# Kernel optimization log

Measured on AMD Instinct MI355X. Metric: run time of the kernel, lower is better.

## Reference

```python
import jax, jax.numpy as jnp
import numpy as np

N_EXPERTS = 6
TOP_K = 2
AUX_COEFF = 0.01
W_SCALE = 0.02  # keep activations in a sane range with random weights


def setup_inputs() -> dict:
    key = jax.random.key(0)
    k1, k2, k3, k4 = jax.random.split(key, 4)
    B, T, D, H = 4, 2048, 1024, 4096
    x = jax.random.normal(k1, (B, T, D), dtype=jnp.float32)
    w_router = jax.random.normal(k2, (D, N_EXPERTS), dtype=jnp.float32) * W_SCALE
    w1 = jax.random.normal(k3, (N_EXPERTS, D, H), dtype=jnp.float32) * W_SCALE
    w2 = jax.random.normal(k4, (N_EXPERTS, H, D), dtype=jnp.float32) * W_SCALE
    return {"x": x, "w_router": w_router, "w1": w1, "w2": w2}


def reference(x, w_router, w1, w2):
    B, T, D = x.shape
    x_flat = x.reshape(-1, D)                              # (N, D)
    router_logits = x_flat @ w_router                      # (N, E)
    router_probs = jax.nn.softmax(router_logits, axis=-1)
    top_probs, top_idx = jax.lax.top_k(router_probs, TOP_K)  # (N, K)
    top_probs = top_probs / jnp.sum(top_probs, axis=-1, keepdims=True)
    # combine weights per (token, expert): sum over k slots hitting expert e
    onehot = jax.nn.one_hot(top_idx, N_EXPERTS, dtype=x.dtype)  # (N, K, E)
    comb = jnp.einsum('nke,nk->ne', onehot, top_probs)          # (N, E)
    out = jnp.zeros_like(x_flat)
    for e in range(N_EXPERTS):
        h = jax.nn.gelu(x_flat @ w1[e], approximate=False)      # (N, H)
        out = out + comb[:, e:e + 1] * (h @ w2[e])              # (N, D)
    tokens_per_expert = jnp.mean(router_probs, axis=0)          # (E,)
    uniform = jnp.full_like(tokens_per_expert, 1.0 / N_EXPERTS)
    aux_loss = AUX_COEFF * jnp.mean((tokens_per_expert - uniform) ** 2)
    return out.reshape(B, T, D), aux_loss
```

## Files before the change

kernel.cpp:

```cpp
#include <hip/hip_runtime.h>

#define N_TOK 8192
#define DDIM  1024
#define HDIM  4096
#define NEXP  6
#define RBLOCKS (N_TOK / 4)
#define SBLOCKS 32

typedef unsigned short ushort_t;
typedef __bf16 bf16_t;
typedef bf16_t bf16x8 __attribute__((ext_vector_type(8)));
typedef float f32x4 __attribute__((ext_vector_type(4)));

typedef const __attribute__((address_space(1))) void* gptr_t;
typedef __attribute__((address_space(3))) void* lptr_t;

__device__ __forceinline__ void g2l16(const void* g, void* l) {
    __builtin_amdgcn_global_load_lds((gptr_t)g, (lptr_t)l, 16, 0, 0);
}

__device__ __forceinline__ ushort_t f2bf(float f) {
    unsigned int u = __float_as_uint(f);
    unsigned int r = (u + 0x7FFFu + ((u >> 16) & 1u)) >> 16;
    return (ushort_t)r;
}

__global__ void convert_x_kernel(const float* __restrict__ x, ushort_t* __restrict__ xb) {
    size_t i = (size_t)(blockIdx.x * 256 + threadIdx.x) * 8;
    float4 a = *(const float4*)(x + i);
    float4 b = *(const float4*)(x + i + 4);
    union { ushort_t u[8]; uint4 v; } o;
    o.u[0] = f2bf(a.x); o.u[1] = f2bf(a.y); o.u[2] = f2bf(a.z); o.u[3] = f2bf(a.w);
    o.u[4] = f2bf(b.x); o.u[5] = f2bf(b.y); o.u[6] = f2bf(b.z); o.u[7] = f2bf(b.w);
    *(uint4*)(xb + i) = o.v;
}

__global__ void transpose_bf16_kernel(const float* __restrict__ src, ushort_t* __restrict__ dst,
                                      int R, int C) {
    __shared__ float tile[32][33];
    size_t msz = (size_t)R * C;
    src += (size_t)blockIdx.z * msz;
    dst += (size_t)blockIdx.z * msz;
    int c0 = blockIdx.x * 32, r0 = blockIdx.y * 32;
    int tx = threadIdx.x & 31, ty = threadIdx.x >> 5;
#pragma unroll
    for (int i = 0; i < 4; ++i)
        tile[ty + 8 * i][tx] = src[(size_t)(r0 + ty + 8 * i) * C + c0 + tx];
    __syncthreads();
#pragma unroll
    for (int i = 0; i < 4; ++i)
        dst[(size_t)(c0 + ty + 8 * i) * R + r0 + tx] = f2bf(tile[tx][ty + 8 * i]);
}

__global__ void router_kernel(const float* __restrict__ x, const float* __restrict__ wr,
                              int* __restrict__ tok_e, float* __restrict__ tok_w,
                              float* __restrict__ part_p, int* __restrict__ part_c) {
    __shared__ float bsum[NEXP];
    __shared__ int bcnt[NEXP];
    int wid = threadIdx.x >> 6, l = threadIdx.x & 63;
    if (threadIdx.x < NEXP) { bsum[threadIdx.x] = 0.f; bcnt[threadIdx.x] = 0; }
    __syncthreads();
    int t = blockIdx.x * 4 + wid;
    const float* xr = x + (size_t)t * DDIM;
    float acc[NEXP] = {0.f, 0.f, 0.f, 0.f, 0.f, 0.f};
#pragma unroll
    for (int c = 0; c < 4; ++c) {
        int k0 = c * 256 + l * 4;
        float4 xv = *(const float4*)(xr + k0);
        float wv[24];
#pragma unroll
        for (int q = 0; q < 6; ++q)
            *(float4*)(wv + 4 * q) = *(const float4*)(wr + (size_t)k0 * NEXP + 4 * q);
        float xa[4] = {xv.x, xv.y, xv.z, xv.w};
#pragma unroll
        for (int r = 0; r < 4; ++r)
#pragma unroll
            for (int e = 0; e < NEXP; ++e) acc[e] += xa[r] * wv[r * NEXP + e];
    }
#pragma unroll
    for (int e = 0; e < NEXP; ++e)
#pragma unroll
        for (int d = 32; d >= 1; d >>= 1) acc[e] += __shfl_xor(acc[e], d);
    if (l == 0) {
        float m = acc[0];
#pragma unroll
        for (int e = 1; e < NEXP; ++e) m = fmaxf(m, acc[e]);
        float p[NEXP], s = 0.f;
#pragma unroll
        for (int e = 0; e < NEXP; ++e) { p[e] = expf(acc[e] - m); s += p[e]; }
        float inv = 1.0f / s;
#pragma unroll
        for (int e = 0; e < NEXP; ++e) p[e] *= inv;
        int i1 = 0; float b1 = p[0];
#pragma unroll
        for (int e = 1; e < NEXP; ++e) if (p[e] > b1) { b1 = p[e]; i1 = e; }
        int i2 = -1; float b2 = -1.f;
#pragma unroll
        for (int e = 0; e < NEXP; ++e) if (e != i1 && p[e] > b2) { b2 = p[e]; i2 = e; }
        float swn = 1.0f / (b1 + b2);
        tok_e[2 * t] = i1; tok_e[2 * t + 1] = i2;
        tok_w[2 * t] = b1 * swn; tok_w[2 * t + 1] = b2 * swn;
        atomicAdd(&bcnt[i1], 1);
        atomicAdd(&bcnt[i2], 1);
#pragma unroll
        for (int e = 0; e < NEXP; ++e) atomicAdd(&bsum[e], p[e]);
    }
    __syncthreads();
    if (threadIdx.x < NEXP) {
        part_p[(size_t)blockIdx.x * NEXP + threadIdx.x] = bsum[threadIdx.x];
        part_c[(size_t)blockIdx.x * NEXP + threadIdx.x] = bcnt[threadIdx.x];
    }
}

__global__ void finalize_kernel(const float* __restrict__ part_p, const int* __restrict__ part_c,
                                int* __restrict__ counts, int* __restrict__ offs,
                                float* __restrict__ aux_out) {
    __shared__ float redp[NEXP][4];
    __shared__ int redc[NEXP][4];
    int tid = threadIdx.x, wid = tid >> 6, l = tid & 63;
    float myp[NEXP] = {0.f, 0.f, 0.f, 0.f, 0.f, 0.f};
    int myc[NEXP] = {0, 0, 0, 0, 0, 0};
    for (int b = tid; b < RBLOCKS; b += 256) {
#pragma unroll
        for (int e = 0; e < NEXP; ++e) {
            myp[e] += part_p[(size_t)b * NEXP + e];
            myc[e] += part_c[(size_t)b * NEXP + e];
        }
    }
#pragma unroll
    for (int e = 0; e < NEXP; ++e) {
#pragma unroll
        for (int d = 32; d >= 1; d >>= 1) {
            myp[e] += __shfl_xor(myp[e], d);
            myc[e] += __shfl_xor(myc[e], d);
        }
        if (l == 0) { redp[e][wid] = myp[e]; redc[e][wid] = myc[e]; }
    }
    __syncthreads();
    if (tid == 0) {
        int o = 0;
        float s = 0.f;
        for (int e = 0; e < NEXP; ++e) {
            int c = redc[e][0] + redc[e][1] + redc[e][2] + redc[e][3];
            float ps = redp[e][0] + redp[e][1] + redp[e][2] + redp[e][3];
            counts[e] = c;
            offs[e] = o;
            o += c;
            float d = ps / (float)N_TOK - (1.0f / 6.0f);
            s += d * d;
        }
        offs[NEXP] = o;
        aux_out[0] = 0.01f * (s / 6.0f);
    }
}

__global__ void scatter_kernel(const int* __restrict__ tok_e, const float* __restrict__ tok_w,
                               const int* __restrict__ offs, int* __restrict__ cursors,
                               int* __restrict__ slot_token, float* __restrict__ slot_w) {
    __shared__ int lcnt[NEXP], lbase[NEXP];
    int tid = threadIdx.x;
    if (tid < NEXP) lcnt[tid] = 0;
    __syncthreads();
    int t = blockIdx.x * 256 + tid;
    int e0 = tok_e[2 * t], e1 = tok_e[2 * t + 1];
    int r0 = atomicAdd(&lcnt[e0], 1);
    int r1 = atomicAdd(&lcnt[e1], 1);
    __syncthreads();
    if (tid < NEXP) lbase[tid] = atomicAdd(&cursors[tid], lcnt[tid]);
    __syncthreads();
    int i0 = offs[e0] + lbase[e0] + r0;
    slot_token[i0] = t; slot_w[i0] = tok_w[2 * t];
    int i1 = offs[e1] + lbase[e1] + r1;
    slot_token[i1] = t; slot_w[i1] = tok_w[2 * t + 1];
}

template <int LAYER>
__global__ __launch_bounds__(256, 2)
void moe_gemm_kernel(const ushort_t* __restrict__ A, const ushort_t* __restrict__ Bt,
                     ushort_t* __restrict__ Hout, float* __restrict__ Out,
                     const int* __restrict__ slot_token, const float* __restrict__ slot_w,
                     const int* __restrict__ offs, const int* __restrict__ counts) {
    constexpr int Kd = (LAYER == 1) ? DDIM : HDIM;
    constexpr int Nd = (LAYER == 1) ? HDIM : DDIM;
    const int e = blockIdx.z;
    const int cnt = counts[e];
    const int mbase = blockIdx.y * 128;
    if (mbase >= cnt) return;
    const int nbase = blockIdx.x * 128;
    const int off = offs[e];
    const ushort_t* Bte = Bt + (size_t)e * ((size_t)Nd * Kd);

    __shared__ __align__(16) ushort_t lds[8192];

    const int tid = threadIdx.x;
    const int wid = tid >> 6, l = tid & 63;

    size_t aoff[2], boff[2];
#pragma unroll
    for (int j = 0; j < 2; ++j) {
        int row = (j * 256 + tid) >> 2;
        int slot = tid & 3;
        int kg = slot ^ ((row >> 1) & 3);
        int lr = mbase + row;
        int lrc = lr < cnt - 1 ? lr : cnt - 1;
        size_t arow;
        if (LAYER == 1) arow = (size_t)slot_token[off + lrc] * DDIM;
        else            arow = (size_t)(off + lrc) * HDIM;
        aoff[j] = arow + (size_t)kg * 8;
        boff[j] = (size_t)(nbase + row) * Kd + (size_t)kg * 8;
    }
    ushort_t* ldsA0 = lds + wid * 512;
    ushort_t* ldsA1 = lds + 2048 + wid * 512;
    ushort_t* ldsB0 = lds + 4096 + wid * 512;
    ushort_t* ldsB1 = lds + 6144 + wid * 512;

    const int lm = l & 15, kg = l >> 4;
    const char* ldsAb = (const char*)lds;
    const char* ldsBb = (const char*)(lds + 4096);
    const int wm = (wid & 1) * 64, wn = (wid >> 1) * 64;
    int arowb[4], browb[4];
#pragma unroll
    for (int f = 0; f < 4; ++f) {
        int ar = wm + f * 16 + lm;
        arowb[f] = ar * 64 + ((kg ^ ((ar >> 1) & 3)) << 4);
        int br = wn + f * 16 + lm;
        browb[f] = br * 64 + ((kg ^ ((br >> 1) & 3)) << 4);
    }

    f32x4 acc[4][4] = {};

    for (int kt = 0; kt < Kd; kt += 32) {
        g2l16(A + aoff[0] + kt, ldsA0);
        g2l16(A + aoff[1] + kt, ldsA1);
        g2l16(Bte + boff[0] + kt, ldsB0);
        g2l16(Bte + boff[1] + kt, ldsB1);
        __syncthreads();
        bf16x8 af[4], bfv[4];
#pragma unroll
        for (int f = 0; f < 4; ++f) {
            af[f]  = *(const bf16x8*)(ldsAb + arowb[f]);
            bfv[f] = *(const bf16x8*)(ldsBb + browb[f]);
        }
#pragma unroll
        for (int i = 0; i < 4; ++i)
#pragma unroll
            for (int jj = 0; jj < 4; ++jj)
                acc[i][jj] = __builtin_amdgcn_mfma_f32_16x16x32_bf16(af[i], bfv[jj], acc[i][jj], 0, 0, 0);
        __syncthreads();
    }

    if (LAYER == 1) {
#pragma unroll
        for (int i = 0; i < 4; ++i) {
#pragma unroll
            for (int r = 0; r < 4; ++r) {
                int row = wm + i * 16 + kg * 4 + r;
                int grow = mbase + row;
                if (grow < cnt) {
                    size_t hbase = (size_t)(off + grow) * HDIM + nbase + wn + lm;
#pragma unroll
                    for (int jj = 0; jj < 4; ++jj) {
                        float v = acc[i][jj][r];
                        float g = 0.5f * v * (1.0f + erff(v * 0.70710678118654752f));
                        Hout[hbase + jj * 16] = f2bf(g);
                    }
                }
            }
        }
    } else {
#pragma unroll
        for (int i = 0; i < 4; ++i) {
#pragma unroll
            for (int r = 0; r < 4; ++r) {
                int row = wm + i * 16 + kg * 4 + r;
                int grow = mbase + row;
                if (grow < cnt) {
                    int si = off + grow;
                    int tok = slot_token[si];
                    float wgt = slot_w[si];
                    float* obase = Out + (size_t)tok * DDIM + nbase + wn + lm;
#pragma unroll
                    for (int jj = 0; jj < 4; ++jj)
                        atomicAdd(obase + jj * 16, wgt * acc[i][jj][r]);
                }
            }
        }
    }
}

extern "C" void kernel_launch(void* const* d_in, const int* in_sizes, int n_in,
                              void* d_out, int out_size, void* d_ws, size_t ws_size,
                              hipStream_t stream) {
    const float* x  = (const float*)d_in[0];
    const float* wr = (const float*)d_in[1];
    const float* w1 = (const float*)d_in[2];
    const float* w2 = (const float*)d_in[3];
    float* out = (float*)d_out;

    char* ws = (char*)d_ws;
    size_t o = 0;
    ushort_t* xb   = (ushort_t*)(ws + o); o += (size_t)N_TOK * DDIM * 2;
    ushort_t* w1t  = (ushort_t*)(ws + o); o += (size_t)NEXP * HDIM * DDIM * 2;
    ushort_t* w2t  = (ushort_t*)(ws + o); o += (size_t)NEXP * DDIM * HDIM * 2;
    ushort_t* hbuf = (ushort_t*)(ws + o); o += (size_t)2 * N_TOK * HDIM * 2;
    int*   tok_e   = (int*)(ws + o);   o += (size_t)N_TOK * 2 * 4;
    float* tok_w   = (float*)(ws + o); o += (size_t)N_TOK * 2 * 4;
    int*   slot_token = (int*)(ws + o);   o += (size_t)2 * N_TOK * 4;
    float* slot_w     = (float*)(ws + o); o += (size_t)2 * N_TOK * 4;
    float* part_p  = (float*)(ws + o); o += (size_t)RBLOCKS * NEXP * 4;
    int*   part_c  = (int*)(ws + o);   o += (size_t)RBLOCKS * NEXP * 4;
    int*   counts  = (int*)(ws + o);   o += 32;
    int*   cursors = (int*)(ws + o);   o += 32;
    int*   offs    = (int*)(ws + o);   o += 32;

    hipMemsetAsync(d_out, 0, (size_t)out_size * sizeof(float), stream);
    hipMemsetAsync(cursors, 0, 32, stream);

    convert_x_kernel<<<dim3(N_TOK * DDIM / 8 / 256), 256, 0, stream>>>(x, xb);
    transpose_bf16_kernel<<<dim3(HDIM / 32, DDIM / 32, NEXP), 256, 0, stream>>>(w1, w1t, DDIM, HDIM);
    transpose_bf16_kernel<<<dim3(DDIM / 32, HDIM / 32, NEXP), 256, 0, stream>>>(w2, w2t, HDIM, DDIM);
    router_kernel<<<dim3(RBLOCKS), 256, 0, stream>>>(x, wr, tok_e, tok_w, part_p, part_c);
    finalize_kernel<<<dim3(1), 256, 0, stream>>>(part_p, part_c, counts, offs, out + (size_t)N_TOK * DDIM);
    scatter_kernel<<<dim3(SBLOCKS), 256, 0, stream>>>(tok_e, tok_w, offs, cursors, slot_token, slot_w);
    moe_gemm_kernel<1><<<dim3(HDIM / 128, N_TOK / 128, NEXP), 256, 0, stream>>>(
        xb, w1t, hbuf, nullptr, slot_token, slot_w, offs, counts);
    moe_gemm_kernel<2><<<dim3(DDIM / 128, N_TOK / 128, NEXP), 256, 0, stream>>>(
        hbuf, w2t, nullptr, out, slot_token, slot_w, offs, counts);
}
```

Before: 567.5 us.

## Fuse x bf16 conversion into router, remap GEMM tiles per XCD, tanh GELU

The separate fp32-to-bf16 conversion kernel for x is removed and done inside the router kernel, which already reads x, saving one full pass over the activations. The MoE GEMM remaps block ids so each XCD processes a contiguous range of tiles, aiming at better L2 locality for shared A/B panels. The exact erf GELU is replaced by the tanh approximation written as a sigmoid with a fast exp, reducing epilogue cost at the price of a small numerical deviation.

Result: slower. 1.086 ms (+91.3%).

```diff
diff --git a/kernel.cpp b/kernel.cpp
--- a/kernel.cpp
+++ b/kernel.cpp
@@ -23,16 +23,6 @@
     unsigned int u = __float_as_uint(f);
     unsigned int r = (u + 0x7FFFu + ((u >> 16) & 1u)) >> 16;
     return (ushort_t)r;
-}
-
-__global__ void convert_x_kernel(const float* __restrict__ x, ushort_t* __restrict__ xb) {
-    size_t i = (size_t)(blockIdx.x * 256 + threadIdx.x) * 8;
-    float4 a = *(const float4*)(x + i);
-    float4 b = *(const float4*)(x + i + 4);
-    union { ushort_t u[8]; uint4 v; } o;
-    o.u[0] = f2bf(a.x); o.u[1] = f2bf(a.y); o.u[2] = f2bf(a.z); o.u[3] = f2bf(a.w);
-    o.u[4] = f2bf(b.x); o.u[5] = f2bf(b.y); o.u[6] = f2bf(b.z); o.u[7] = f2bf(b.w);
-    *(uint4*)(xb + i) = o.v;
 }
 
 __global__ void transpose_bf16_kernel(const float* __restrict__ src, ushort_t* __restrict__ dst,
@@ -53,6 +43,7 @@
 }
 
 __global__ void router_kernel(const float* __restrict__ x, const float* __restrict__ wr,
+                              ushort_t* __restrict__ xb,
                               int* __restrict__ tok_e, float* __restrict__ tok_w,
                               float* __restrict__ part_p, int* __restrict__ part_c) {
     __shared__ float bsum[NEXP];
@@ -62,11 +53,15 @@
     __syncthreads();
     int t = blockIdx.x * 4 + wid;
     const float* xr = x + (size_t)t * DDIM;
+    ushort_t* xbr = xb + (size_t)t * DDIM;
     float acc[NEXP] = {0.f, 0.f, 0.f, 0.f, 0.f, 0.f};
 #pragma unroll
     for (int c = 0; c < 4; ++c) {
         int k0 = c * 256 + l * 4;
         float4 xv = *(const float4*)(xr + k0);
+        union { ushort_t u[4]; uint2 v; } ob;
+        ob.u[0] = f2bf(xv.x); ob.u[1] = f2bf(xv.y); ob.u[2] = f2bf(xv.z); ob.u[3] = f2bf(xv.w);
+        *(uint2*)(xbr + k0) = ob.v;
         float wv[24];
 #pragma unroll
         for (int q = 0; q < 6; ++q)
@@ -181,14 +176,21 @@
                      const int* __restrict__ slot_token, const float* __restrict__ slot_w,
                      const int* __restrict__ offs, const int* __restrict__ counts) {
     constexpr int Kd = (LAYER == 1) ? DDIM : HDIM;
-    constexpr int Nd = (LAYER == 1) ? HDIM : DDIM;
     const int e = blockIdx.z;
     const int cnt = counts[e];
-    const int mbase = blockIdx.y * 128;
+
+    const int NXb = gridDim.x;
+    const int nwg = NXb * gridDim.y;
+    int f = blockIdx.x + NXb * blockIdx.y;
+    int q8 = nwg >> 3, r8 = nwg & 7;
+    int xcd = f & 7, lo = f >> 3;
+    int wg = (xcd < r8 ? xcd * (q8 + 1) : r8 * (q8 + 1) + (xcd - r8) * q8) + lo;
+    const int mbase = (wg / NXb) * 128;
     if (mbase >= cnt) return;
-    const int nbase = blockIdx.x * 128;
+    const int nbase = (wg % NXb) * 128;
+
     const int off = offs[e];
-    const ushort_t* Bte = Bt + (size_t)e * ((size_t)Nd * Kd);
+    const ushort_t* Bte = Bt + (size_t)e * ((size_t)((LAYER == 1) ? HDIM : DDIM) * Kd);
 
     __shared__ __align__(16) ushort_t lds[8192];
 
@@ -220,11 +222,11 @@
     const int wm = (wid & 1) * 64, wn = (wid >> 1) * 64;
     int arowb[4], browb[4];
 #pragma unroll
-    for (int f = 0; f < 4; ++f) {
-        int ar = wm + f * 16 + lm;
-        arowb[f] = ar * 64 + ((kg ^ ((ar >> 1) & 3)) << 4);
-        int br = wn + f * 16 + lm;
-        browb[f] = br * 64 + ((kg ^ ((br >> 1) & 3)) << 4);
+    for (int fr = 0; fr < 4; ++fr) {
+        int ar = wm + fr * 16 + lm;
+        arowb[fr] = ar * 64 + ((kg ^ ((ar >> 1) & 3)) << 4);
+        int br = wn + fr * 16 + lm;
+        browb[fr] = br * 64 + ((kg ^ ((br >> 1) & 3)) << 4);
     }
 
     f32x4 acc[4][4] = {};
@@ -237,9 +239,9 @@
         __syncthreads();
         bf16x8 af[4], bfv[4];
 #pragma unroll
-        for (int f = 0; f < 4; ++f) {
-            af[f]  = *(const bf16x8*)(ldsAb + arowb[f]);
-            bfv[f] = *(const bf16x8*)(ldsBb + browb[f]);
+        for (int fr = 0; fr < 4; ++fr) {
+            af[fr]  = *(const bf16x8*)(ldsAb + arowb[fr]);
+            bfv[fr] = *(const bf16x8*)(ldsBb + browb[fr]);
         }
 #pragma unroll
         for (int i = 0; i < 4; ++i)
@@ -261,7 +263,8 @@
 #pragma unroll
                     for (int jj = 0; jj < 4; ++jj) {
                         float v = acc[i][jj][r];
-                        float g = 0.5f * v * (1.0f + erff(v * 0.70710678118654752f));
+                        float u = -1.5957691216f * v * (1.0f + 0.044715f * v * v);
+                        float g = v / (1.0f + __expf(u));
                         Hout[hbase + jj * 16] = f2bf(g);
                     }
                 }
@@ -316,10 +319,9 @@
     hipMemsetAsync(d_out, 0, (size_t)out_size * sizeof(float), stream);
     hipMemsetAsync(cursors, 0, 32, stream);
 
-    convert_x_kernel<<<dim3(N_TOK * DDIM / 8 / 256), 256, 0, stream>>>(x, xb);
+    router_kernel<<<dim3(RBLOCKS), 256, 0, stream>>>(x, wr, xb, tok_e, tok_w, part_p, part_c);
     transpose_bf16_kernel<<<dim3(HDIM / 32, DDIM / 32, NEXP), 256, 0, stream>>>(w1, w1t, DDIM, HDIM);
     transpose_bf16_kernel<<<dim3(DDIM / 32, HDIM / 32, NEXP), 256, 0, stream>>>(w2, w2t, HDIM, DDIM);
-    router_kernel<<<dim3(RBLOCKS), 256, 0, stream>>>(x, wr, tok_e, tok_w, part_p, part_c);
     finalize_kernel<<<dim3(1), 256, 0, stream>>>(part_p, part_c, counts, offs, out + (size_t)N_TOK * DDIM);
     scatter_kernel<<<dim3(SBLOCKS), 256, 0, stream>>>(tok_e, tok_w, offs, cursors, slot_token, slot_w);
     moe_gemm_kernel<1><<<dim3(HDIM / 128, N_TOK / 128, NEXP), 256, 0, stream>>>(
```
